# Kernel optimization log

Hardware: AMD Instinct MI355X
Metric: run time of the kernel (lower is better)

Reference implementation:

```python
import jax, jax.numpy as jnp
import numpy as np

_C, _H, _DH = 256, 8, 32
_B, _S, _L = 2, 4, 1024


def setup_inputs() -> dict:
    key = jax.random.key(0)
    ks = jax.random.split(key, 12)
    sc = 1.0 / np.sqrt(_C)
    return {
        "x": jax.random.normal(ks[0], (_B * _S, _L, _C), jnp.float32),
        "bulk_map": jax.random.normal(ks[1], (_B, 1, _L, _L), jnp.float32),
        "Wq": jax.random.normal(ks[2], (_C, _C), jnp.float32) * sc,
        "bq": jnp.zeros((_C,), jnp.float32),
        "Wk": jax.random.normal(ks[3], (_C, _C), jnp.float32) * sc,
        "bk": jnp.zeros((_C,), jnp.float32),
        "Wv": jax.random.normal(ks[4], (_C, _C), jnp.float32) * sc,
        "bv": jnp.zeros((_C,), jnp.float32),
        "Wo": jax.random.normal(ks[5], (_C, _C), jnp.float32) * sc,
        "bo": jnp.zeros((_C,), jnp.float32),
        "conv_w": jax.random.normal(ks[6], (_H,), jnp.float32) * 0.1,  # 1x1 Conv2d(1->H)
        "conv_b": jnp.zeros((_H,), jnp.float32),
        "gate_w": jax.random.normal(ks[7], (_H, _DH, _DH), jnp.float32) * (1.0 / np.sqrt(_DH)),
        "gate_b": jnp.zeros((_H, _DH), jnp.float32),
        "ln_g": jnp.ones((_C,), jnp.float32),
        "ln_b": jnp.zeros((_C,), jnp.float32),
        "B": _B, "S": _S, "L": _L,
    }


def reference(x, bulk_map, Wq, bq, Wk, bk, Wv, bv, Wo, bo,
              conv_w, conv_b, gate_w, gate_b, ln_g, ln_b, B, S, L):
    BS, _, C = x.shape
    H, DH, _ = gate_w.shape
    # projections -> (BS, H, L, DH)
    def split_heads(t):
        return t.reshape(BS, L, H, DH).transpose(0, 2, 1, 3)
    q = split_heads(x @ Wq.T + bq)
    k = split_heads(x @ Wk.T + bk)
    v = split_heads(x @ Wv.T + bv)
    scores = jnp.einsum('bhqd,bhkd->bhqk', q, k) / (DH ** 0.5)  # (BS,H,L,L)
    # 1x1 conv bias from bulk map: (B,H,L,L), broadcast over S tracks
    bias = conv_w[None, :, None, None] * bulk_map + conv_b[None, :, None, None]
    scores = scores.reshape(B, S, H, L, L) + bias[:, None]
    attn = jax.nn.softmax(scores, axis=-1).reshape(BS, H, L, L)
    out = jnp.einsum('bhqk,bhkd->bhqd', attn, v)  # (BS,H,L,DH)
    gate = jax.nn.sigmoid(jnp.einsum('hcd,bhld->bhlc', gate_w, out)
                          + gate_b[None, :, None, :])
    out = out * gate
    out = out.transpose(0, 2, 1, 3).reshape(BS, L, C) @ Wo.T + bo
    y = x + out
    mu = y.mean(-1, keepdims=True)
    var = y.var(-1, keepdims=True)
    return (y - mu) / jnp.sqrt(var + 1e-5) * ln_g + ln_b
```

## Files before the change

### kernel.cpp

```cpp
#include <hip/hip_runtime.h>
#include <hip/hip_bf16.h>

#define C_ 256
#define H_ 8
#define DH_ 32
#define L_ 1024

typedef __bf16 bf16x8_t __attribute__((ext_vector_type(8)));
typedef float f32x4_t __attribute__((ext_vector_type(4)));
typedef float f32x16_t __attribute__((ext_vector_type(16)));

union V16 {
    uint4 u4;
    bf16x8_t b8;
    f32x4_t f4;
    unsigned u[4];
};

__device__ __forceinline__ unsigned cvt_pk(float lo, float hi) {
    unsigned r;
    asm volatile("v_cvt_pk_bf16_f32 %0, %1, %2" : "=v"(r) : "v"(lo), "v"(hi));
    return r;
}

__device__ __forceinline__ f32x4_t mfma16(bf16x8_t a, bf16x8_t b, f32x4_t c) {
    return __builtin_amdgcn_mfma_f32_16x16x32_bf16(a, b, c, 0, 0, 0);
}
__device__ __forceinline__ f32x16_t mfma32(bf16x8_t a, bf16x8_t b, f32x16_t c) {
    return __builtin_amdgcn_mfma_f32_32x32x16_bf16(a, b, c, 0, 0, 0);
}

__device__ __forceinline__ void pl32swap(unsigned& a, unsigned& b) {
    asm volatile("v_permlane32_swap_b32 %0, %1" : "+v"(a), "+v"(b));
}

__device__ __forceinline__ unsigned short f2bf(float f) {
    unsigned u = __float_as_uint(f);
    u += 0x7fffu + ((u >> 16) & 1u);
    return (unsigned short)(u >> 16);
}
__device__ __forceinline__ float bfup(unsigned short u) {
    return __uint_as_float((unsigned)u << 16);
}
__device__ __forceinline__ float bflo(unsigned u) { return __uint_as_float(u << 16); }
__device__ __forceinline__ float bfhi(unsigned u) { return __uint_as_float(u & 0xffff0000u); }
__device__ __forceinline__ float ex2(float x) { return __builtin_amdgcn_exp2f(x); }

#define LOG2E_F 1.4426950408889634f

__device__ __forceinline__ float tmax16(const f32x16_t& v) {
    float a = fmaxf(fmaxf(v[0], v[1]), fmaxf(v[2], v[3]));
    float b = fmaxf(fmaxf(v[4], v[5]), fmaxf(v[6], v[7]));
    float c = fmaxf(fmaxf(v[8], v[9]), fmaxf(v[10], v[11]));
    float d = fmaxf(fmaxf(v[12], v[13]), fmaxf(v[14], v[15]));
    return fmaxf(fmaxf(a, b), fmaxf(c, d));
}
__device__ __forceinline__ float tsum16(const f32x16_t& v) {
    float a = (v[0] + v[1]) + (v[2] + v[3]);
    float b = (v[4] + v[5]) + (v[6] + v[7]);
    float c = (v[8] + v[9]) + (v[10] + v[11]);
    float d = (v[12] + v[13]) + (v[14] + v[15]);
    return (a + b) + (c + d);
}

__global__ __launch_bounds__(256) void conv_bf16(
    const float* __restrict__ x,
    const float* __restrict__ Wq, const float* __restrict__ Wk,
    const float* __restrict__ Wv, const float* __restrict__ Wo,
    unsigned short* __restrict__ xb, unsigned short* __restrict__ wb)
{
    int ysel = blockIdx.y;
    const float* src; unsigned short* dst; int n4;
    if (ysel == 0) { src = x; dst = xb; n4 = 524288; }
    else {
        src = (ysel == 1) ? Wq : (ysel == 2) ? Wk : (ysel == 3) ? Wv : Wo;
        dst = wb + (ysel - 1) * 65536; n4 = 16384;
    }
    int i = blockIdx.x * 256 + threadIdx.x;
    if (i >= n4) return;
    float4 v = ((const float4*)src)[i];
    ushort4 o;
    o.x = f2bf(v.x); o.y = f2bf(v.y); o.z = f2bf(v.z); o.w = f2bf(v.w);
    ((ushort4*)dst)[i] = o;
}

__global__ __launch_bounds__(256) void transpose_bulk(
    const float* __restrict__ bulk, unsigned short* __restrict__ bulkT)
{
    __shared__ unsigned short tile[32][33];
    const int b = blockIdx.z;
    const int q0 = blockIdx.x * 32, kv0 = blockIdx.y * 32;
    const int t = threadIdx.x;
    const int c = t & 31, r = t >> 5;
    const float* src = bulk + (size_t)b * 1048576;
#pragma unroll
    for (int p = 0; p < 4; ++p) {
        int q = r + p * 8;
        tile[c][q] = f2bf(src[(size_t)(q0 + q) * 1024 + kv0 + c]);
    }
    __syncthreads();
    unsigned short* dst = bulkT + (size_t)b * 1048576;
#pragma unroll
    for (int p = 0; p < 4; ++p) {
        int kv = r + p * 8;
        dst[(size_t)(kv0 + kv) * 1024 + q0 + c] = tile[kv][c];
    }
}

__global__ __launch_bounds__(256) void qkv_mfma(
    const unsigned short* __restrict__ xb, const unsigned short* __restrict__ wb,
    const float* __restrict__ bq, const float* __restrict__ bk, const float* __restrict__ bv,
    unsigned short* __restrict__ qws, unsigned short* __restrict__ kws,
    unsigned short* __restrict__ vws)
{
    const int t = threadIdx.x;
    const int lane = t & 63, w = t >> 6;
    const int r = lane & 15, g = lane >> 4;
    const int m0 = blockIdx.x * 64 + (w >> 1) * 32;
    const int n0g = blockIdx.y * 64 + (w & 1) * 32;
    const int z = n0g >> 8, nl = n0g & 255;

    const uint4* ap = (const uint4*)xb;
    const uint4* bp = (const uint4*)(wb + z * 65536);

    f32x4_t acc[2][2] = {};
#pragma unroll
    for (int kt = 0; kt < 8; ++kt) {
        V16 w0, w1, x0, x1;
        w0.u4 = bp[(nl + r) * 32 + kt * 4 + g];
        w1.u4 = bp[(nl + 16 + r) * 32 + kt * 4 + g];
        x0.u4 = ap[(m0 + r) * 32 + kt * 4 + g];
        x1.u4 = ap[(m0 + 16 + r) * 32 + kt * 4 + g];
        acc[0][0] = mfma16(w0.b8, x0.b8, acc[0][0]);
        acc[0][1] = mfma16(w0.b8, x1.b8, acc[0][1]);
        acc[1][0] = mfma16(w1.b8, x0.b8, acc[1][0]);
        acc[1][1] = mfma16(w1.b8, x1.b8, acc[1][1]);
    }

    const float* bias = (z == 0) ? bq : (z == 1) ? bk : bv;
    unsigned short* dst = (z == 0) ? qws : (z == 1) ? kws : vws;
    const float sc = (z == 0) ? (0.17677669529663687f * LOG2E_F) : 1.0f;
#pragma unroll
    for (int wi = 0; wi < 2; ++wi) {
        f32x4_t b4 = *(const f32x4_t*)&bias[nl + wi * 16 + g * 4];
        int nc = nl + wi * 16 + g * 4;
        int h = nc >> 5, d0 = nc & 31;
#pragma unroll
        for (int mi = 0; mi < 2; ++mi) {
            int tok = m0 + mi * 16 + r;
            int bs = tok >> 10, l = tok & 1023;
            float v0 = (acc[wi][mi][0] + b4[0]) * sc;
            float v1 = (acc[wi][mi][1] + b4[1]) * sc;
            float v2 = (acc[wi][mi][2] + b4[2]) * sc;
            float v3 = (acc[wi][mi][3] + b4[3]) * sc;
            uint2 st;
            st.x = cvt_pk(v0, v1);
            st.y = cvt_pk(v2, v3);
            *(uint2*)&dst[((size_t)((bs * H_ + h) * L_ + l)) * DH_ + d0] = st;
        }
    }
}

__global__ __launch_bounds__(256) void transpose_v(const unsigned short* __restrict__ vws,
                                                   unsigned short* __restrict__ vT)
{
    __shared__ unsigned short tile[32][264];
    int hb = blockIdx.y;
    int l0 = blockIdx.x * 256;
    int t = threadIdx.x;
    const unsigned* src = (const unsigned*)(vws + (size_t)hb * 32768) + l0 * 16;
    for (int i = t; i < 4096; i += 256) {
        int l = i >> 4, d2 = i & 15;
        unsigned u = src[i];
        tile[d2 * 2][l]     = (unsigned short)(u & 0xffffu);
        tile[d2 * 2 + 1][l] = (unsigned short)(u >> 16);
    }
    __syncthreads();
    unsigned* dst = (unsigned*)(vT + (size_t)hb * 32768);
    int d = t >> 3, seg = (t & 7) * 32;
#pragma unroll
    for (int j = 0; j < 16; ++j) {
        int l = seg + j * 2;
        unsigned u = (unsigned)tile[d][l] | ((unsigned)tile[d][l + 1] << 16);
        dst[d * 512 + (l0 + l) / 2] = u;
    }
}

__global__ __launch_bounds__(256, 4) void attn_mfma(
    const unsigned short* __restrict__ qws, const unsigned short* __restrict__ kws,
    const unsigned short* __restrict__ vT, const unsigned short* __restrict__ bulkT,
    const float* __restrict__ conv_w, const float* __restrict__ conv_b,
    const float* __restrict__ gate_w, const float* __restrict__ gate_b,
    unsigned short* __restrict__ ogb)
{
    __shared__ unsigned olds[3][64][9];
    __shared__ float2 mlds[3][64];

    const int t = threadIdx.x;
    const int lane = t & 63;
    const int la = lane & 31, hi = lane >> 5;
    const int qr = t >> 6;
    const int s = blockIdx.y;
    const int h = blockIdx.z & 7, b = blockIdx.z >> 3;
    const int hb = (b * 4 + s) * 8 + h;
    const int q0 = blockIdx.x * 32;

    const uint4* kp = (const uint4*)(kws + (size_t)hb * 32768);
    const uint4* qp = (const uint4*)(qws + (size_t)hb * 32768);
    const uint4* vp = (const uint4*)(vT  + (size_t)hb * 32768) + la * 128 + hi + qr * 32;
    const float cw2 = conv_w[h] * LOG2E_F, cb2 = conv_b[h] * LOG2E_F;

    bf16x8_t qb0, qb1;
    { V16 m; m.u4 = qp[(q0 + la) * 4 + hi];     qb0 = m.b8; }
    { V16 m; m.u4 = qp[(q0 + la) * 4 + 2 + hi]; qb1 = m.b8; }

    f32x16_t o = {};
    float mst = -3.0e38f, lst = 0.f;

    const int kvbase = qr * 256;
    for (int kt = 0; kt < 4; ++kt) {
        const int kvA = kvbase + kt * 64;
        bf16x8_t kA0, kA1, kB0, kB1;
        { V16 m; m.u4 = kp[(kvA + la) * 4 + hi];          kA0 = m.b8; }
        { V16 m; m.u4 = kp[(kvA + la) * 4 + 2 + hi];      kA1 = m.b8; }
        { V16 m; m.u4 = kp[(kvA + 32 + la) * 4 + hi];     kB0 = m.b8; }
        { V16 m; m.u4 = kp[(kvA + 32 + la) * 4 + 2 + hi]; kB1 = m.b8; }
        V16 v0, v1, v2, v3;
        v0.u4 = vp[kt * 8];
        v1.u4 = vp[kt * 8 + 2];
        v2.u4 = vp[kt * 8 + 4];
        v3.u4 = vp[kt * 8 + 6];
        const unsigned short* bpT = bulkT + (size_t)b * 1048576
                                  + (size_t)(kvA + 4 * hi) * 1024 + q0 + la;
        f32x16_t accA, accB;
#pragma unroll
        for (int a = 0; a < 4; ++a)
#pragma unroll
            for (int i = 0; i < 4; ++i) {
                accA[4 * a + i] = cw2 * bfup(bpT[(8 * a + i) * 1024]) + cb2;
                accB[4 * a + i] = cw2 * bfup(bpT[(8 * a + i) * 1024 + 32768]) + cb2;
            }
        __builtin_amdgcn_s_setprio(1);
        accA = mfma32(kA0, qb0, accA);
        accA = mfma32(kA1, qb1, accA);
        accB = mfma32(kB0, qb0, accB);
        accB = mfma32(kB1, qb1, accB);
        __builtin_amdgcn_s_setprio(0);

        float pmax = fmaxf(tmax16(accA), tmax16(accB));
        pmax = fmaxf(pmax, __shfl_xor(pmax, 32, 64));
        if (!__all(pmax <= mst + 8.0f)) {
            float mnew = fmaxf(mst, pmax);
            float scl = ex2(mst - mnew);
            mst = mnew; lst *= scl;
            o *= scl;
        }
#pragma unroll
        for (int e = 0; e < 16; ++e) {
            accA[e] = ex2(accA[e] - mst);
            accB[e] = ex2(accB[e] - mst);
        }
        float psum = tsum16(accA) + tsum16(accB);
        psum += __shfl_xor(psum, 32, 64);
        lst += psum;

        unsigned pkA[4][2], pkB[4][2];
#pragma unroll
        for (int a = 0; a < 4; ++a) {
            pkA[a][0] = cvt_pk(accA[4 * a], accA[4 * a + 1]);
            pkA[a][1] = cvt_pk(accA[4 * a + 2], accA[4 * a + 3]);
            pkB[a][0] = cvt_pk(accB[4 * a], accB[4 * a + 1]);
            pkB[a][1] = cvt_pk(accB[4 * a + 2], accB[4 * a + 3]);
        }
        pl32swap(pkA[0][0], pkA[1][0]); pl32swap(pkA[0][1], pkA[1][1]);
        pl32swap(pkA[2][0], pkA[3][0]); pl32swap(pkA[2][1], pkA[3][1]);
        pl32swap(pkB[0][0], pkB[1][0]); pl32swap(pkB[0][1], pkB[1][1]);
        pl32swap(pkB[2][0], pkB[3][0]); pl32swap(pkB[2][1], pkB[3][1]);
        V16 pA0, pA1, pB0, pB1;
        pA0.u[0] = pkA[0][0]; pA0.u[1] = pkA[0][1]; pA0.u[2] = pkA[1][0]; pA0.u[3] = pkA[1][1];
        pA1.u[0] = pkA[2][0]; pA1.u[1] = pkA[2][1]; pA1.u[2] = pkA[3][0]; pA1.u[3] = pkA[3][1];
        pB0.u[0] = pkB[0][0]; pB0.u[1] = pkB[0][1]; pB0.u[2] = pkB[1][0]; pB0.u[3] = pkB[1][1];
        pB1.u[0] = pkB[2][0]; pB1.u[1] = pkB[2][1]; pB1.u[2] = pkB[3][0]; pB1.u[3] = pkB[3][1];
        __builtin_amdgcn_s_setprio(1);
        o = mfma32(v0.b8, pA0.b8, o);
        o = mfma32(v1.b8, pA1.b8, o);
        o = mfma32(v2.b8, pB0.b8, o);
        o = mfma32(v3.b8, pB1.b8, o);
        __builtin_amdgcn_s_setprio(0);
    }

    if (qr != 0) {
        unsigned* dl = &olds[qr - 1][lane][0];
#pragma unroll
        for (int i = 0; i < 8; ++i)
            dl[i] = cvt_pk(o[2 * i], o[2 * i + 1]);
        mlds[qr - 1][lane] = make_float2(mst, lst);
    }
    __syncthreads();
    if (qr == 0) {
        float2 m1 = mlds[0][lane];
        float2 m2 = mlds[1][lane];
        float2 m3 = mlds[2][lane];
        float M = fmaxf(fmaxf(mst, m1.x), fmaxf(m2.x, m3.x));
        float w0 = ex2(mst - M), w1 = ex2(m1.x - M);
        float w2 = ex2(m2.x - M), w3 = ex2(m3.x - M);
        float li = 1.0f / (lst * w0 + m1.y * w1 + m2.y * w2 + m3.y * w3);
        w0 *= li; w1 *= li; w2 *= li; w3 *= li;
        const unsigned* p1 = &olds[0][lane][0];
        const unsigned* p2 = &olds[1][lane][0];
        const unsigned* p3 = &olds[2][lane][0];
        float of[16];
#pragma unroll
        for (int i = 0; i < 8; ++i) {
            unsigned u1 = p1[i], u2 = p2[i], u3 = p3[i];
            of[2 * i]     = o[2 * i] * w0     + bflo(u1) * w1 + bflo(u2) * w2 + bflo(u3) * w3;
            of[2 * i + 1] = o[2 * i + 1] * w0 + bfhi(u1) * w1 + bfhi(u2) * w2 + bfhi(u3) * w3;
        }

        bf16x8_t ga0, ga1;
        {
            const float* gw = gate_w + (size_t)(h * 32 + la) * 32 + hi * 8;
            V16 m;
            f32x4_t a0 = *(const f32x4_t*)gw, a1 = *(const f32x4_t*)(gw + 4);
            m.u[0] = cvt_pk(a0[0], a0[1]); m.u[1] = cvt_pk(a0[2], a0[3]);
            m.u[2] = cvt_pk(a1[0], a1[1]); m.u[3] = cvt_pk(a1[2], a1[3]);
            ga0 = m.b8;
            f32x4_t a2 = *(const f32x4_t*)(gw + 16), a3 = *(const f32x4_t*)(gw + 20);
            m.u[0] = cvt_pk(a2[0], a2[1]); m.u[1] = cvt_pk(a2[2], a2[3]);
            m.u[2] = cvt_pk(a3[0], a3[1]); m.u[3] = cvt_pk(a3[2], a3[3]);
            ga1 = m.b8;
        }
        unsigned pk[4][2];
#pragma unroll
        for (int a = 0; a < 4; ++a) {
            pk[a][0] = cvt_pk(of[4 * a], of[4 * a + 1]);
            pk[a][1] = cvt_pk(of[4 * a + 2], of[4 * a + 3]);
        }
        pl32swap(pk[0][0], pk[1][0]); pl32swap(pk[0][1], pk[1][1]);
        pl32swap(pk[2][0], pk[3][0]); pl32swap(pk[2][1], pk[3][1]);
        V16 oB0, oB1;
        oB0.u[0] = pk[0][0]; oB0.u[1] = pk[0][1]; oB0.u[2] = pk[1][0]; oB0.u[3] = pk[1][1];
        oB1.u[0] = pk[2][0]; oB1.u[1] = pk[2][1]; oB1.u[2] = pk[3][0]; oB1.u[3] = pk[3][1];
        f32x16_t gacc = {};
        gacc = mfma32(ga0, oB0.b8, gacc);
        gacc = mfma32(ga1, oB1.b8, gacc);

#pragma unroll
        for (int a = 0; a < 4; ++a) {
            f32x4_t gb4 = *(const f32x4_t*)(gate_b + h * 32 + 8 * a + 4 * hi);
#pragma unroll
            for (int i = 0; i < 4; ++i) {
                float garg = gacc[4 * a + i] + gb4[i];
                float sg = 1.0f / (1.0f + ex2(-garg * LOG2E_F));
                of[4 * a + i] *= sg;
            }
        }

        unsigned* ogp = (unsigned*)ogb + ((size_t)(hb * 1024 + q0 + la)) * 16;
#pragma unroll
        for (int a = 0; a < 4; ++a) {
            uint2 st;
            st.x = cvt_pk(of[4 * a], of[4 * a + 1]);
            st.y = cvt_pk(of[4 * a + 2], of[4 * a + 3]);
            *(uint2*)&ogp[4 * a + 2 * hi] = st;
        }
    }
}

__global__ __launch_bounds__(512) void proj_ln_mfma(
    const unsigned short* __restrict__ ogb, const float* __restrict__ x,
    const unsigned short* __restrict__ wob, const float* __restrict__ bo,
    const float* __restrict__ ln_g, const float* __restrict__ ln_b,
    float* __restrict__ out)
{
    __shared__ float s1l[8][16];
    __shared__ float s2l[8][16];
    const int t = threadIdx.x;
    const int lane = t & 63, w = t >> 6;
    const int r = lane & 15, g = lane >> 4;
    const int m0 = blockIdx.x * 16;
    const int bs = m0 >> 10, l0 = m0 & 1023;
    const int n0 = w * 32;

    const uint4* ap = (const uint4*)ogb;
    const uint4* bp = (const uint4*)wob;

    f32x4_t acc[2] = {};
#pragma unroll
    for (int kt = 0; kt < 8; ++kt) {
        V16 a0, b0, b1;
        a0.u4 = ap[((size_t)(bs * 8 + kt) * 1024 + l0 + r) * 4 + g];
        b0.u4 = bp[(n0 + r) * 32 + kt * 4 + g];
        b1.u4 = bp[(n0 + 16 + r) * 32 + kt * 4 + g];
        acc[0] = mfma16(a0.b8, b0.b8, acc[0]);
        acc[1] = mfma16(a0.b8, b1.b8, acc[1]);
    }

    float bo0 = bo[n0 + r], bo1 = bo[n0 + 16 + r];
#pragma unroll
    for (int e = 0; e < 4; ++e) {
        int m = m0 + g * 4 + e;
        acc[0][e] += bo0 + x[(size_t)m * 256 + n0 + r];
        acc[1][e] += bo1 + x[(size_t)m * 256 + n0 + 16 + r];
    }
#pragma unroll
    for (int e = 0; e < 4; ++e) {
        float sm = acc[0][e] + acc[1][e];
        float sq = acc[0][e] * acc[0][e] + acc[1][e] * acc[1][e];
        sm += __shfl_xor(sm, 1, 64); sq += __shfl_xor(sq, 1, 64);
        sm += __shfl_xor(sm, 2, 64); sq += __shfl_xor(sq, 2, 64);
        sm += __shfl_xor(sm, 4, 64); sq += __shfl_xor(sq, 4, 64);
        sm += __shfl_xor(sm, 8, 64); sq += __shfl_xor(sq, 8, 64);
        if (r == 0) { s1l[w][g * 4 + e] = sm; s2l[w][g * 4 + e] = sq; }
    }
    __syncthreads();

    float g0 = ln_g[n0 + r], g1 = ln_g[n0 + 16 + r];
    float b0 = ln_b[n0 + r], b1 = ln_b[n0 + 16 + r];
#pragma unroll
    for (int e = 0; e < 4; ++e) {
        int mloc = g * 4 + e;
        float sm = 0.f, sq = 0.f;
#pragma unroll
        for (int wv = 0; wv < 8; ++wv) { sm += s1l[wv][mloc]; sq += s2l[wv][mloc]; }
        float mu = sm * (1.0f / 256.0f);
        float var = sq * (1.0f / 256.0f) - mu * mu;
        float rs = rsqrtf(var + 1e-5f);
        int m = m0 + mloc;
        out[(size_t)m * 256 + n0 + r]      = (acc[0][e] - mu) * rs * g0 + b0;
        out[(size_t)m * 256 + n0 + 16 + r] = (acc[1][e] - mu) * rs * g1 + b1;
    }
}

extern "C" void kernel_launch(void* const* d_in, const int* in_sizes, int n_in,
                              void* d_out, int out_size, void* d_ws, size_t ws_size,
                              hipStream_t stream)
{
    (void)in_sizes; (void)n_in; (void)out_size; (void)ws_size;
    const float* x      = (const float*)d_in[0];
    const float* bulk   = (const float*)d_in[1];
    const float* Wq     = (const float*)d_in[2];
    const float* bq     = (const float*)d_in[3];
    const float* Wk     = (const float*)d_in[4];
    const float* bk     = (const float*)d_in[5];
    const float* Wv     = (const float*)d_in[6];
    const float* bv     = (const float*)d_in[7];
    const float* Wo     = (const float*)d_in[8];
    const float* bo     = (const float*)d_in[9];
    const float* conv_w = (const float*)d_in[10];
    const float* conv_b = (const float*)d_in[11];
    const float* gate_w = (const float*)d_in[12];
    const float* gate_b = (const float*)d_in[13];
    const float* ln_g   = (const float*)d_in[14];
    const float* ln_b   = (const float*)d_in[15];
    float* out = (float*)d_out;

    char* ws = (char*)d_ws;
    unsigned short* xb  = (unsigned short*)ws;
    unsigned short* wb  = (unsigned short*)(ws + (4u << 20));
    unsigned short* qws = (unsigned short*)(ws + (4u << 20) + (512u << 10));
    unsigned short* kws = qws + 2097152;
    unsigned short* vws = qws + 4194304;
    unsigned short* vT  = qws + 6291456;
    unsigned short* bulkT = (unsigned short*)(ws + (20u << 20) + (512u << 10));
    unsigned short* ogb = vws;
    unsigned short* wob = wb + 3 * 65536;

    conv_bf16<<<dim3(2048, 5), 256, 0, stream>>>(x, Wq, Wk, Wv, Wo, xb, wb);
    transpose_bulk<<<dim3(32, 32, 2), 256, 0, stream>>>(bulk, bulkT);
    qkv_mfma<<<dim3(128, 12), 256, 0, stream>>>(xb, wb, bq, bk, bv, qws, kws, vws);
    transpose_v<<<dim3(4, 64), 256, 0, stream>>>(vws, vT);
    attn_mfma<<<dim3(32, 4, 16), 256, 0, stream>>>(qws, kws, vT, bulkT, conv_w, conv_b,
                                                   gate_w, gate_b, ogb);
    proj_ln_mfma<<<512, 512, 0, stream>>>(ogb, x, wob, bo, ln_g, ln_b, out);
}
```

Measured before the change: 97.33 us.

## Merge prep kernels, write V transposed from QKV GEMM, pack bulk bias layout

```diff
diff --git a/kernel.cpp b/kernel.cpp
--- a/kernel.cpp
+++ b/kernel.cpp
@@ -63,36 +63,37 @@
     return (a + b) + (c + d);
 }
 
-__global__ __launch_bounds__(256) void conv_bf16(
+__global__ __launch_bounds__(256) void conv_prep(
     const float* __restrict__ x,
     const float* __restrict__ Wq, const float* __restrict__ Wk,
     const float* __restrict__ Wv, const float* __restrict__ Wo,
-    unsigned short* __restrict__ xb, unsigned short* __restrict__ wb)
+    const float* __restrict__ bulk,
+    unsigned short* __restrict__ xb, unsigned short* __restrict__ wb,
+    unsigned short* __restrict__ bulkT)
 {
     int ysel = blockIdx.y;
-    const float* src; unsigned short* dst; int n4;
-    if (ysel == 0) { src = x; dst = xb; n4 = 524288; }
-    else {
-        src = (ysel == 1) ? Wq : (ysel == 2) ? Wk : (ysel == 3) ? Wv : Wo;
-        dst = wb + (ysel - 1) * 65536; n4 = 16384;
-    }
-    int i = blockIdx.x * 256 + threadIdx.x;
-    if (i >= n4) return;
-    float4 v = ((const float4*)src)[i];
-    ushort4 o;
-    o.x = f2bf(v.x); o.y = f2bf(v.y); o.z = f2bf(v.z); o.w = f2bf(v.w);
-    ((ushort4*)dst)[i] = o;
-}
-
-__global__ __launch_bounds__(256) void transpose_bulk(
-    const float* __restrict__ bulk, unsigned short* __restrict__ bulkT)
-{
+    int t = threadIdx.x;
+    if (ysel < 5) {
+        const float* src; unsigned short* dst; int n4;
+        if (ysel == 0) { src = x; dst = xb; n4 = 524288; }
+        else {
+            src = (ysel == 1) ? Wq : (ysel == 2) ? Wk : (ysel == 3) ? Wv : Wo;
+            dst = wb + (ysel - 1) * 65536; n4 = 16384;
+        }
+        int i = blockIdx.x * 256 + t;
+        if (i >= n4) return;
+        float4 v = ((const float4*)src)[i];
+        ushort4 o;
+        o.x = f2bf(v.x); o.y = f2bf(v.y); o.z = f2bf(v.z); o.w = f2bf(v.w);
+        ((ushort4*)dst)[i] = o;
+        return;
+    }
     __shared__ unsigned short tile[32][33];
-    const int b = blockIdx.z;
-    const int q0 = blockIdx.x * 32, kv0 = blockIdx.y * 32;
-    const int t = threadIdx.x;
-    const int c = t & 31, r = t >> 5;
+    int bx = blockIdx.x;
+    int b = bx >> 10, rem = bx & 1023;
+    int q0 = (rem >> 5) * 32, kv0 = (rem & 31) * 32;
     const float* src = bulk + (size_t)b * 1048576;
+    int c = t & 31, r = t >> 5;
 #pragma unroll
     for (int p = 0; p < 4; ++p) {
         int q = r + p * 8;
@@ -100,18 +101,17 @@
     }
     __syncthreads();
     unsigned short* dst = bulkT + (size_t)b * 1048576;
-#pragma unroll
-    for (int p = 0; p < 4; ++p) {
-        int kv = r + p * 8;
-        dst[(size_t)(kv0 + kv) * 1024 + q0 + c] = tile[kv][c];
-    }
+    ushort4 w;
+    w.x = tile[4 * r + 0][c]; w.y = tile[4 * r + 1][c];
+    w.z = tile[4 * r + 2][c]; w.w = tile[4 * r + 3][c];
+    *(ushort4*)&dst[((size_t)((kv0 >> 2) + r) * 1024 + q0 + c) * 4] = w;
 }
 
 __global__ __launch_bounds__(256) void qkv_mfma(
     const unsigned short* __restrict__ xb, const unsigned short* __restrict__ wb,
     const float* __restrict__ bq, const float* __restrict__ bk, const float* __restrict__ bv,
     unsigned short* __restrict__ qws, unsigned short* __restrict__ kws,
-    unsigned short* __restrict__ vws)
+    unsigned short* __restrict__ vT)
 {
     const int t = threadIdx.x;
     const int lane = t & 63, w = t >> 6;
@@ -138,8 +138,26 @@
     }
 
     const float* bias = (z == 0) ? bq : (z == 1) ? bk : bv;
-    unsigned short* dst = (z == 0) ? qws : (z == 1) ? kws : vws;
     const float sc = (z == 0) ? (0.17677669529663687f * LOG2E_F) : 1.0f;
+    if (z == 2) {
+#pragma unroll
+        for (int wi = 0; wi < 2; ++wi) {
+            f32x4_t b4 = *(const f32x4_t*)&bias[nl + wi * 16 + g * 4];
+            int nc = nl + wi * 16 + g * 4;
+            int h = nc >> 5, d0 = nc & 31;
+#pragma unroll
+            for (int mi = 0; mi < 2; ++mi) {
+                int tok = m0 + mi * 16 + r;
+                int bs = tok >> 10, l = tok & 1023;
+                unsigned short* vbase = vT + (size_t)(bs * H_ + h) * 32768 + l;
+#pragma unroll
+                for (int e = 0; e < 4; ++e)
+                    vbase[(d0 + e) * 1024] = f2bf(acc[wi][mi][e] + b4[e]);
+            }
+        }
+        return;
+    }
+    unsigned short* dst = (z == 0) ? qws : kws;
 #pragma unroll
     for (int wi = 0; wi < 2; ++wi) {
         f32x4_t b4 = *(const f32x4_t*)&bias[nl + wi * 16 + g * 4];
@@ -161,31 +179,6 @@
     }
 }
 
-__global__ __launch_bounds__(256) void transpose_v(const unsigned short* __restrict__ vws,
-                                                   unsigned short* __restrict__ vT)
-{
-    __shared__ unsigned short tile[32][264];
-    int hb = blockIdx.y;
-    int l0 = blockIdx.x * 256;
-    int t = threadIdx.x;
-    const unsigned* src = (const unsigned*)(vws + (size_t)hb * 32768) + l0 * 16;
-    for (int i = t; i < 4096; i += 256) {
-        int l = i >> 4, d2 = i & 15;
-        unsigned u = src[i];
-        tile[d2 * 2][l]     = (unsigned short)(u & 0xffffu);
-        tile[d2 * 2 + 1][l] = (unsigned short)(u >> 16);
-    }
-    __syncthreads();
-    unsigned* dst = (unsigned*)(vT + (size_t)hb * 32768);
-    int d = t >> 3, seg = (t & 7) * 32;
-#pragma unroll
-    for (int j = 0; j < 16; ++j) {
-        int l = seg + j * 2;
-        unsigned u = (unsigned)tile[d][l] | ((unsigned)tile[d][l + 1] << 16);
-        dst[d * 512 + (l0 + l) / 2] = u;
-    }
-}
-
 __global__ __launch_bounds__(256, 4) void attn_mfma(
     const unsigned short* __restrict__ qws, const unsigned short* __restrict__ kws,
     const unsigned short* __restrict__ vT, const unsigned short* __restrict__ bulkT,
@@ -208,6 +201,7 @@
     const uint4* kp = (const uint4*)(kws + (size_t)hb * 32768);
     const uint4* qp = (const uint4*)(qws + (size_t)hb * 32768);
     const uint4* vp = (const uint4*)(vT  + (size_t)hb * 32768) + la * 128 + hi + qr * 32;
+    const unsigned short* bpT = bulkT + (size_t)b * 1048576 + (size_t)(q0 + la) * 4;
     const float cw2 = conv_w[h] * LOG2E_F, cb2 = conv_b[h] * LOG2E_F;
 
     bf16x8_t qb0, qb1;
@@ -220,6 +214,7 @@
     const int kvbase = qr * 256;
     for (int kt = 0; kt < 4; ++kt) {
         const int kvA = kvbase + kt * 64;
+        const int kvb = kvA >> 2;
         bf16x8_t kA0, kA1, kB0, kB1;
         { V16 m; m.u4 = kp[(kvA + la) * 4 + hi];          kA0 = m.b8; }
         { V16 m; m.u4 = kp[(kvA + la) * 4 + 2 + hi];      kA1 = m.b8; }
@@ -230,16 +225,20 @@
         v1.u4 = vp[kt * 8 + 2];
         v2.u4 = vp[kt * 8 + 4];
         v3.u4 = vp[kt * 8 + 6];
-        const unsigned short* bpT = bulkT + (size_t)b * 1048576
-                                  + (size_t)(kvA + 4 * hi) * 1024 + q0 + la;
         f32x16_t accA, accB;
 #pragma unroll
-        for (int a = 0; a < 4; ++a)
-#pragma unroll
-            for (int i = 0; i < 4; ++i) {
-                accA[4 * a + i] = cw2 * bfup(bpT[(8 * a + i) * 1024]) + cb2;
-                accB[4 * a + i] = cw2 * bfup(bpT[(8 * a + i) * 1024 + 32768]) + cb2;
-            }
+        for (int a = 0; a < 4; ++a) {
+            ushort4 ua = *(const ushort4*)(bpT + (size_t)(kvb + 2 * a + hi) * 4096);
+            ushort4 ub = *(const ushort4*)(bpT + (size_t)(kvb + 8 + 2 * a + hi) * 4096);
+            accA[4 * a + 0] = cw2 * bfup(ua.x) + cb2;
+            accA[4 * a + 1] = cw2 * bfup(ua.y) + cb2;
+            accA[4 * a + 2] = cw2 * bfup(ua.z) + cb2;
+            accA[4 * a + 3] = cw2 * bfup(ua.w) + cb2;
+            accB[4 * a + 0] = cw2 * bfup(ub.x) + cb2;
+            accB[4 * a + 1] = cw2 * bfup(ub.y) + cb2;
+            accB[4 * a + 2] = cw2 * bfup(ub.z) + cb2;
+            accB[4 * a + 3] = cw2 * bfup(ub.w) + cb2;
+        }
         __builtin_amdgcn_s_setprio(1);
         accA = mfma32(kA0, qb0, accA);
         accA = mfma32(kA1, qb1, accA);
@@ -456,20 +455,17 @@
     float* out = (float*)d_out;
 
     char* ws = (char*)d_ws;
-    unsigned short* xb  = (unsigned short*)ws;
-    unsigned short* wb  = (unsigned short*)(ws + (4u << 20));
-    unsigned short* qws = (unsigned short*)(ws + (4u << 20) + (512u << 10));
-    unsigned short* kws = qws + 2097152;
-    unsigned short* vws = qws + 4194304;
-    unsigned short* vT  = qws + 6291456;
-    unsigned short* bulkT = (unsigned short*)(ws + (20u << 20) + (512u << 10));
-    unsigned short* ogb = vws;
-    unsigned short* wob = wb + 3 * 65536;
-
-    conv_bf16<<<dim3(2048, 5), 256, 0, stream>>>(x, Wq, Wk, Wv, Wo, xb, wb);
-    transpose_bulk<<<dim3(32, 32, 2), 256, 0, stream>>>(bulk, bulkT);
-    qkv_mfma<<<dim3(128, 12), 256, 0, stream>>>(xb, wb, bq, bk, bv, qws, kws, vws);
-    transpose_v<<<dim3(4, 64), 256, 0, stream>>>(vws, vT);
+    unsigned short* xb    = (unsigned short*)ws;
+    unsigned short* wb    = (unsigned short*)(ws + (4u << 20));
+    unsigned short* qws   = (unsigned short*)(ws + (4u << 20) + (512u << 10));
+    unsigned short* kws   = qws + 2097152;
+    unsigned short* vT    = qws + 4194304;
+    unsigned short* bulkT = qws + 6291456;
+    unsigned short* ogb   = xb;
+    unsigned short* wob   = wb + 3 * 65536;
+
+    conv_prep<<<dim3(2048, 6), 256, 0, stream>>>(x, Wq, Wk, Wv, Wo, bulk, xb, wb, bulkT);
+    qkv_mfma<<<dim3(128, 12), 256, 0, stream>>>(xb, wb, bq, bk, bv, qws, kws, vT);
     attn_mfma<<<dim3(32, 4, 16), 256, 0, stream>>>(qws, kws, vT, bulkT, conv_w, conv_b,
                                                    gate_w, gate_b, ogb);
     proj_ln_mfma<<<512, 512, 0, stream>>>(ogb, x, wob, bo, ln_g, ln_b, out);
```

Result: faster. 86.25 us (-11.4%).
